# Kernel tuning notes

Hardware: AMD Instinct MI355X
Metric: run time of the kernel (lower is better)

Reference implementation:

```python
import jax, jax.numpy as jnp
import numpy as np

N = 50000
IN, HID, OUT, HEADS = 128, 64, 64, 4


def seg_softmax(logits, seg, num):
    # softmax over edges grouped by destination node; logits [E, H]
    m = jax.ops.segment_max(logits, seg, num_segments=num)
    e = jnp.exp(logits - m[seg])
    s = jax.ops.segment_sum(e, seg, num_segments=num)
    return e / (s[seg] + 1e-16)


def gat_conv(x, src, dst, W, a_s, a_d, b, heads, concat):
    n = x.shape[0]
    h = (x @ W.T).reshape(n, heads, -1)           # [N, H, C]
    alpha_src = jnp.einsum('nhc,hc->nh', h, a_s)   # per-node src score
    alpha_dst = jnp.einsum('nhc,hc->nh', h, a_d)
    logits = jax.nn.leaky_relu(alpha_src[src] + alpha_dst[dst], 0.2)  # [E, H]
    alpha = seg_softmax(logits, dst, n)
    out = jax.ops.segment_sum(alpha[:, :, None] * h[src], dst, num_segments=n)  # [N, H, C]
    out = out.reshape(n, -1) if concat else out.mean(axis=1)
    return out + b


def setup_inputs():
    key = jax.random.key(0)
    ks = jax.random.split(key, 16)
    x = jax.random.normal(ks[0], (N, IN), dtype=jnp.float32)
    edge_index = jax.random.randint(ks[1], (2, 800000), 0, N, dtype=jnp.int64)

    def glorot(k, shape):
        fan = shape[-1]
        return jax.random.normal(k, shape, dtype=jnp.float32) / jnp.sqrt(jnp.float32(fan))

    d = {"x": x, "edge_index": edge_index}
    # layer 1: IN -> HID, HEADS heads, concat
    d["W1"] = glorot(ks[2], (HEADS * HID, IN))
    d["as1"] = glorot(ks[3], (HEADS, HID))
    d["ad1"] = glorot(ks[4], (HEADS, HID))
    d["b1"] = jnp.zeros((HEADS * HID,), jnp.float32)
    # layer 2: HID*HEADS -> HID, HEADS heads, concat
    d["W2"] = glorot(ks[5], (HEADS * HID, HEADS * HID))
    d["as2"] = glorot(ks[6], (HEADS, HID))
    d["ad2"] = glorot(ks[7], (HEADS, HID))
    d["b2"] = jnp.zeros((HEADS * HID,), jnp.float32)
    # layer 3: HID*HEADS -> OUT, 1 head
    d["W3"] = glorot(ks[8], (OUT, HEADS * HID))
    d["as3"] = glorot(ks[9], (1, OUT))
    d["ad3"] = glorot(ks[10], (1, OUT))
    d["b3"] = jnp.zeros((OUT,), jnp.float32)
    return d


def reference(x, edge_index, W1, as1, ad1, b1, W2, as2, ad2, b2, W3, as3, ad3, b3):
    # PyG GATConv adds self-loops by default
    loops = jnp.arange(N, dtype=edge_index.dtype)
    src = jnp.concatenate([edge_index[0], loops])
    dst = jnp.concatenate([edge_index[1], loops])

    h = jax.nn.relu(gat_conv(x, src, dst, W1, as1, ad1, b1, HEADS, True))
    h = jax.nn.relu(gat_conv(h, src, dst, W2, as2, ad2, b2, HEADS, True))
    out = gat_conv(h, src, dst, W3, as3, ad3, b3, 1, True)
    return out
```

## Files before the change

kernel.cpp:

```cpp
#include <hip/hip_runtime.h>
#include <hip/hip_bf16.h>
#include <math.h>


typedef __bf16 bf16x8 __attribute__((ext_vector_type(8)));
typedef float f32x4 __attribute__((ext_vector_type(4)));
typedef _Float16 half8v __attribute__((ext_vector_type(8)));

#define QINV 2048.0f
#define QDQ  4.8828125e-4f

__device__ __forceinline__ void gload_lds16(const void* g, void* l) {
  __builtin_amdgcn_global_load_lds(
      (const __attribute__((address_space(1))) unsigned int*)g,
      (__attribute__((address_space(3))) unsigned int*)l, 16, 0, 0);
}

__device__ __forceinline__ unsigned int splitf(float a) {
  __hip_bfloat16 h = __float2bfloat16(a);
  float hf = __bfloat162float(h);
  __hip_bfloat16 l = __float2bfloat16(a - hf);
  return (unsigned int)__builtin_bit_cast(unsigned short, h) |
         ((unsigned int)__builtin_bit_cast(unsigned short, l) << 16);
}

__device__ __forceinline__ float leaky02(float l) {
  return (l >= 0.f) ? l : 0.2f * l;
}

__device__ __forceinline__ short quant16(float v) {
  int q = (int)rintf(v * QINV);
  q = q > 32767 ? 32767 : (q < -32768 ? -32768 : q);
  return (short)q;
}


__global__ void init_counts_kernel(int* counts, int n) {
  int i = blockIdx.x * blockDim.x + threadIdx.x;
  if (i < n) counts[i] = 1;
}

__global__ void hist_kernel(const int* __restrict__ dst, int e, int* counts) {
  int i = blockIdx.x * blockDim.x + threadIdx.x;
  if (i < e) atomicAdd(&counts[dst[i]], 1);
}

__global__ __launch_bounds__(1024) void block_sum_kernel(const int* __restrict__ counts,
                                                         int* __restrict__ bsum, int n) {
  __shared__ int red[1024];
  int i = blockIdx.x * 1024 + threadIdx.x;
  red[threadIdx.x] = (i < n) ? counts[i] : 0;
  __syncthreads();
  #pragma unroll
  for (int off = 512; off > 0; off >>= 1) {
    if (threadIdx.x < off) red[threadIdx.x] += red[threadIdx.x + off];
    __syncthreads();
  }
  if (threadIdx.x == 0) bsum[blockIdx.x] = red[0];
}

__global__ void scan_sums_kernel(int* bsum, int nb) {
  int t = threadIdx.x;
  int c = (t < nb) ? bsum[t] : 0;
  int v = c;
  #pragma unroll
  for (int off = 1; off < 64; off <<= 1) {
    int u = __shfl_up(v, off);
    if (t >= off) v += u;
  }
  if (t < nb) bsum[t] = v - c;
}

__global__ __launch_bounds__(1024) void scan_final_kernel(const int* __restrict__ counts,
    const int* __restrict__ bsum, int* __restrict__ offsets, int* __restrict__ cursor, int n) {
  __shared__ int sc[1024];
  int i = blockIdx.x * 1024 + threadIdx.x;
  int c = (i < n) ? counts[i] : 0;
  sc[threadIdx.x] = c;
  __syncthreads();
  for (int off = 1; off < 1024; off <<= 1) {
    int v = 0;
    if (threadIdx.x >= off) v = sc[threadIdx.x - off];
    __syncthreads();
    sc[threadIdx.x] += v;
    __syncthreads();
  }
  int excl = sc[threadIdx.x] - c + bsum[blockIdx.x];
  if (i < n) {
    offsets[i] = excl;
    cursor[i] = excl;
  } else if (i == n) {
    offsets[n] = excl;
  }
}

__global__ void scatter_kernel(const int* __restrict__ src, const int* __restrict__ dst,
                               int e800, int etot, int* cursor, int* __restrict__ ssrc) {
  int i = blockIdx.x * blockDim.x + threadIdx.x;
  if (i >= etot) return;
  int s, d;
  if (i < e800) { s = src[i]; d = dst[i]; }
  else          { s = i - e800; d = s; }
  int pos = atomicAdd(&cursor[d], 1);
  ssrc[pos] = s;
}

__global__ void split_kernel(const float* __restrict__ in, uint4* __restrict__ out, int count4) {
  int i = blockIdx.x * blockDim.x + threadIdx.x;
  if (i >= count4) return;
  float4 v = reinterpret_cast<const float4*>(in)[i];
  uint4 o;
  o.x = splitf(v.x); o.y = splitf(v.y); o.z = splitf(v.z); o.w = splitf(v.w);
  out[i] = o;
}

__global__ void splitW_kernel(const float* __restrict__ W1, const float* __restrict__ W2,
                              const float* __restrict__ W3, uint4* __restrict__ o1,
                              uint4* __restrict__ o2, uint4* __restrict__ o3) {
  int i = blockIdx.x * blockDim.x + threadIdx.x;
  const float* in;
  uint4* out;
  int j;
  if (i < 8192)            { in = W1; out = o1; j = i; }
  else if (i < 8192+16384) { in = W2; out = o2; j = i - 8192; }
  else if (i < 8192+16384+4096) { in = W3; out = o3; j = i - (8192+16384); }
  else return;
  float4 v = reinterpret_cast<const float4*>(in)[j];
  uint4 o;
  o.x = splitf(v.x); o.y = splitf(v.y); o.z = splitf(v.z); o.w = splitf(v.w);
  out[j] = o;
}

template <int KP, int BM, int BN, int WAVES_M, int WAVES_N, int OTOT, int HEADS, bool FP16OUT>
__global__ __launch_bounds__(256) void gemm2_kernel(
    const unsigned short* __restrict__ A, const unsigned short* __restrict__ B,
    void* __restrict__ Cq, const float* __restrict__ a_s, const float* __restrict__ a_d,
    float* __restrict__ asrcO, float* __restrict__ adstO, int M) {
  constexpr int BK = 64;
  constexpr int NK = KP / BK;
  constexpr int MFRAG = BM / WAVES_M / 16;
  constexpr int NFRAG = BN / WAVES_N / 16;
  __shared__ unsigned short As[2][BM * BK];
  __shared__ unsigned short Bs[2][BN * BK];

  const int tid = threadIdx.x;
  const int lane = tid & 63;
  const int wid = tid >> 6;
  const int m0 = blockIdx.x * BM;
  const int o0 = blockIdx.y * BN;

  const int srow = tid >> 3;
  const int scolb = (tid & 7) * 16;
  const int sswz = (srow & 7) << 4;
  const char* aSrc = (const char*)A + (size_t)(m0 + srow) * (KP * 2) + (scolb ^ sswz);
  const char* bSrc = (const char*)B + (size_t)(o0 + srow) * (KP * 2) + (scolb ^ sswz);
  char* aDst0 = (char*)&As[0][0] + wid * 1024;
  char* bDst0 = (char*)&Bs[0][0] + wid * 1024;

  auto stage = [&](int buf, int kt) {
    const size_t ko = (size_t)kt * 128;
    char* ad = aDst0 + buf * (BM * 128);
    #pragma unroll
    for (int i = 0; i < BM / 32; ++i)
      gload_lds16(aSrc + ko + (size_t)i * 32 * (KP * 2), ad + i * 4096);
    char* bd = bDst0 + buf * (BN * 128);
    #pragma unroll
    for (int j = 0; j < BN / 32; ++j)
      gload_lds16(bSrc + ko + (size_t)j * 32 * (KP * 2), bd + j * 4096);
  };

  const int fr = lane & 15;
  const int fg = lane >> 4;
  const int fswz = (fr & 7) << 4;
  const int wm0 = (wid / WAVES_N) * (BM / WAVES_M);
  const int wn0 = (wid % WAVES_N) * (BN / WAVES_N);

  f32x4 acc[MFRAG][NFRAG];
  #pragma unroll
  for (int mi = 0; mi < MFRAG; ++mi)
    #pragma unroll
    for (int ni = 0; ni < NFRAG; ++ni) acc[mi][ni] = (f32x4)0.f;

  stage(0, 0);
  __syncthreads();

  for (int kt = 0; kt < NK; ++kt) {
    const int buf = kt & 1;
    if (kt + 1 < NK) stage(buf ^ 1, kt + 1);
    const char* asB = (const char*)&As[buf][0] + (wm0 + fr) * 128;
    const char* bsB = (const char*)&Bs[buf][0] + (wn0 + fr) * 128;
    #pragma unroll
    for (int kh = 0; kh < 2; ++kh) {
      const int kb = (kh * 64 + fg * 16) ^ fswz;
      bf16x8 af[MFRAG], bfr[NFRAG];
      #pragma unroll
      for (int mi = 0; mi < MFRAG; ++mi)
        af[mi] = *reinterpret_cast<const bf16x8*>(asB + mi * 16 * 128 + kb);
      #pragma unroll
      for (int ni = 0; ni < NFRAG; ++ni)
        bfr[ni] = *reinterpret_cast<const bf16x8*>(bsB + ni * 16 * 128 + kb);
      #pragma unroll
      for (int mi = 0; mi < MFRAG; ++mi)
        #pragma unroll
        for (int ni = 0; ni < NFRAG; ++ni)
          acc[mi][ni] = __builtin_amdgcn_mfma_f32_16x16x32_bf16(af[mi], bfr[ni], acc[mi][ni], 0, 0, 0);
    }
    __syncthreads();
  }

  const int head = (o0 + wn0) >> 6;
  float asl[NFRAG], adl[NFRAG];
  #pragma unroll
  for (int ni = 0; ni < NFRAG; ++ni) {
    int c64 = ni * 16 + fr;
    asl[ni] = a_s[head * 64 + c64];
    adl[ni] = a_d[head * 64 + c64];
  }
  #pragma unroll
  for (int mi = 0; mi < MFRAG; ++mi) {
    #pragma unroll
    for (int r = 0; r < 4; ++r) {
      int row = m0 + wm0 + mi * 16 + fg * 4 + r;
      float ps = 0.f, pd = 0.f;
      #pragma unroll
      for (int ni = 0; ni < NFRAG; ++ni) {
        ps = fmaf(acc[mi][ni][r], asl[ni], ps);
        pd = fmaf(acc[mi][ni][r], adl[ni], pd);
      }
      #pragma unroll
      for (int off = 1; off < 16; off <<= 1) {
        ps += __shfl_xor(ps, off);
        pd += __shfl_xor(pd, off);
      }
      if (row < M) {
        if (fr == 0) {
          asrcO[(size_t)row * HEADS + head] = ps;
          adstO[(size_t)row * HEADS + head] = pd;
        }
        #pragma unroll
        for (int ni = 0; ni < NFRAG; ++ni) {
          size_t ci = (size_t)row * OTOT + o0 + wn0 + ni * 16 + fr;
          if (FP16OUT) ((_Float16*)Cq)[ci] = (_Float16)acc[mi][ni][r];
          else         ((short*)Cq)[ci] = quant16(acc[mi][ni][r]);
        }
      }
    }
  }
}

__global__ __launch_bounds__(256) void aggregate4_kernel(
    const _Float16* __restrict__ hq, const float* __restrict__ asrc,
    const float* __restrict__ adst, const float* __restrict__ bias,
    const int* __restrict__ offsets, const int* __restrict__ ssrc,
    uint4* __restrict__ outp, int n) {
  int wid = threadIdx.x >> 6;
  int lane = threadIdx.x & 63;
  int sub = lane >> 5;
  int hl = lane & 31;
  int node = blockIdx.x * 8 + wid * 2 + sub;
  if (node >= n) return;
  int head = hl >> 3;
  int ch8 = hl * 8;
  float adv = adst[(size_t)node * 4 + head];
  int beg = offsets[node], end = offsets[node + 1];

  float s0 = 0.f, s1 = 0.f, s2 = 0.f, s3 = 0.f;
  float A0[8] = {}, A1[8] = {}, A2[8] = {}, A3[8] = {};
  int e = beg;
  for (; e + 3 < end; e += 4) {
    int c0 = ssrc[e + 0], c1 = ssrc[e + 1], c2 = ssrc[e + 2], c3 = ssrc[e + 3];
    float p0 = __expf(leaky02(asrc[(size_t)c0 * 4 + head] + adv));
    float p1 = __expf(leaky02(asrc[(size_t)c1 * 4 + head] + adv));
    float p2 = __expf(leaky02(asrc[(size_t)c2 * 4 + head] + adv));
    float p3 = __expf(leaky02(asrc[(size_t)c3 * 4 + head] + adv));
    half8v h0 = *reinterpret_cast<const half8v*>(&hq[(size_t)c0 * 256 + ch8]);
    half8v h1 = *reinterpret_cast<const half8v*>(&hq[(size_t)c1 * 256 + ch8]);
    half8v h2 = *reinterpret_cast<const half8v*>(&hq[(size_t)c2 * 256 + ch8]);
    half8v h3 = *reinterpret_cast<const half8v*>(&hq[(size_t)c3 * 256 + ch8]);
    s0 += p0; s1 += p1; s2 += p2; s3 += p3;
    #pragma unroll
    for (int j = 0; j < 8; ++j) {
      A0[j] = fmaf((float)h0[j], p0, A0[j]);
      A1[j] = fmaf((float)h1[j], p1, A1[j]);
      A2[j] = fmaf((float)h2[j], p2, A2[j]);
      A3[j] = fmaf((float)h3[j], p3, A3[j]);
    }
  }
  for (; e < end; ++e) {
    int c0 = ssrc[e];
    float p0 = __expf(leaky02(asrc[(size_t)c0 * 4 + head] + adv));
    half8v h0 = *reinterpret_cast<const half8v*>(&hq[(size_t)c0 * 256 + ch8]);
    s0 += p0;
    #pragma unroll
    for (int j = 0; j < 8; ++j) A0[j] = fmaf((float)h0[j], p0, A0[j]);
  }
  float s = (s0 + s1) + (s2 + s3);
  float A[8];
  #pragma unroll
  for (int j = 0; j < 8; ++j) A[j] = (A0[j] + A1[j]) + (A2[j] + A3[j]);

  float inv = 1.f / (s + 1e-16f);
  float4 bv0 = *reinterpret_cast<const float4*>(&bias[ch8]);
  float4 bv1 = *reinterpret_cast<const float4*>(&bias[ch8 + 4]);
  float o[8];
  o[0] = fmaxf(A[0] * inv + bv0.x, 0.f);
  o[1] = fmaxf(A[1] * inv + bv0.y, 0.f);
  o[2] = fmaxf(A[2] * inv + bv0.z, 0.f);
  o[3] = fmaxf(A[3] * inv + bv0.w, 0.f);
  o[4] = fmaxf(A[4] * inv + bv1.x, 0.f);
  o[5] = fmaxf(A[5] * inv + bv1.y, 0.f);
  o[6] = fmaxf(A[6] * inv + bv1.z, 0.f);
  o[7] = fmaxf(A[7] * inv + bv1.w, 0.f);
  uint4 pk0, pk1;
  pk0.x = splitf(o[0]); pk0.y = splitf(o[1]); pk0.z = splitf(o[2]); pk0.w = splitf(o[3]);
  pk1.x = splitf(o[4]); pk1.y = splitf(o[5]); pk1.z = splitf(o[6]); pk1.w = splitf(o[7]);
  outp[(size_t)node * 64 + hl * 2 + 0] = pk0;
  outp[(size_t)node * 64 + hl * 2 + 1] = pk1;
}

__global__ __launch_bounds__(256) void aggregate1_kernel(
    const short* __restrict__ hq, const float* __restrict__ asrc,
    const float* __restrict__ adst, const float* __restrict__ bias,
    const int* __restrict__ offsets, const int* __restrict__ ssrc,
    float* __restrict__ out, int n) {
  int wid = threadIdx.x >> 6;
  int lane = threadIdx.x & 63;
  int node = blockIdx.x * 4 + wid;
  if (node >= n) return;
  int g = lane >> 4;
  int w = lane & 15;
  float adv = adst[node];
  int beg = offsets[node], end = offsets[node + 1];

  float s = 0.f;
  float4 A = {0, 0, 0, 0};
  int e0 = beg;
  for (; e0 + 3 < end; e0 += 4) {
    int src = ssrc[e0 + g];
    float p = __expf(leaky02(asrc[src] + adv));
    short4 q = *reinterpret_cast<const short4*>(&hq[(size_t)src * 64 + w * 4]);
    s += p;
    A.x += p * (float)q.x; A.y += p * (float)q.y;
    A.z += p * (float)q.z; A.w += p * (float)q.w;
  }
  if (e0 + g < end) {
    int src = ssrc[e0 + g];
    float p = __expf(leaky02(asrc[src] + adv));
    short4 q = *reinterpret_cast<const short4*>(&hq[(size_t)src * 64 + w * 4]);
    s += p;
    A.x += p * (float)q.x; A.y += p * (float)q.y;
    A.z += p * (float)q.z; A.w += p * (float)q.w;
  }
  #pragma unroll
  for (int off = 16; off < 64; off <<= 1) {
    s += __shfl_xor(s, off);
    A.x += __shfl_xor(A.x, off);
    A.y += __shfl_xor(A.y, off);
    A.z += __shfl_xor(A.z, off);
    A.w += __shfl_xor(A.w, off);
  }
  if (g == 0) {
    float inv = QDQ / (s + 1e-16f);
    float4 bv = *reinterpret_cast<const float4*>(&bias[w * 4]);
    float4 o;
    o.x = A.x * inv + bv.x;
    o.y = A.y * inv + bv.y;
    o.z = A.z * inv + bv.z;
    o.w = A.w * inv + bv.w;
    *reinterpret_cast<float4*>(&out[(size_t)node * 64 + w * 4]) = o;
  }
}


extern "C" void kernel_launch(void* const* d_in, const int* in_sizes, int n_in,
                              void* d_out, int out_size, void* d_ws, size_t ws_size,
                              hipStream_t stream) {
  const float* x   = (const float*)d_in[0];
  const int*   ei  = (const int*)d_in[1];
  const float* W1  = (const float*)d_in[2];
  const float* as1 = (const float*)d_in[3];
  const float* ad1 = (const float*)d_in[4];
  const float* b1  = (const float*)d_in[5];
  const float* W2  = (const float*)d_in[6];
  const float* as2 = (const float*)d_in[7];
  const float* ad2 = (const float*)d_in[8];
  const float* b2  = (const float*)d_in[9];
  const float* W3  = (const float*)d_in[10];
  const float* as3 = (const float*)d_in[11];
  const float* ad3 = (const float*)d_in[12];
  const float* b3  = (const float*)d_in[13];
  float* out = (float*)d_out;

  const int n    = in_sizes[0] / 128;
  const int e800 = in_sizes[1] / 2;
  const int etot = e800 + n;
  const int Mpad = 50048;

  char* ws = (char*)d_ws;
  size_t off = 0;
  auto alloc = [&](size_t bytes) -> void* {
    void* p = ws + off;
    off = (off + bytes + 255) & ~(size_t)255;
    return p;
  };
  void*           featQ  = alloc((size_t)Mpad * 256 * 2);
  unsigned short* hsplit = (unsigned short*)alloc((size_t)Mpad * 512 * 2);
  unsigned short* w1s    = (unsigned short*)alloc((size_t)256 * 256 * 2);
  unsigned short* w2s    = (unsigned short*)alloc((size_t)256 * 512 * 2);
  unsigned short* w3s    = (unsigned short*)alloc((size_t)64 * 512 * 2);
  float* asrc    = (float*)alloc((size_t)n * 4 * 4);
  float* adst    = (float*)alloc((size_t)n * 4 * 4);
  int*   ssrc    = (int*)alloc((size_t)etot * 4);
  int*   offsets = (int*)alloc((size_t)(n + 1) * 4);
  int*   cursor  = (int*)alloc((size_t)n * 4);
  int*   counts  = (int*)alloc((size_t)n * 4);
  int*   bsum    = (int*)alloc((size_t)64 * 4);

  const int* esrc = ei;
  const int* edst = ei + e800;
  const int nbScan = (n + 1024) / 1024;

  init_counts_kernel<<<(n + 255) / 256, 256, 0, stream>>>(counts, n);
  hist_kernel<<<(e800 + 255) / 256, 256, 0, stream>>>(edst, e800, counts);
  block_sum_kernel<<<nbScan, 1024, 0, stream>>>(counts, bsum, n);
  scan_sums_kernel<<<1, 64, 0, stream>>>(bsum, nbScan);
  scan_final_kernel<<<nbScan, 1024, 0, stream>>>(counts, bsum, offsets, cursor, n);
  scatter_kernel<<<(etot + 255) / 256, 256, 0, stream>>>(esrc, edst, e800, etot, cursor, ssrc);

  split_kernel<<<(n * 128 / 4 + 255) / 256, 256, 0, stream>>>(x, (uint4*)hsplit, n * 128 / 4);
  splitW_kernel<<<(8192 + 16384 + 4096 + 255) / 256, 256, 0, stream>>>(
      W1, W2, W3, (uint4*)w1s, (uint4*)w2s, (uint4*)w3s);

  const int mBlocks = Mpad / 128;

  gemm2_kernel<256, 128, 128, 2, 2, 256, 4, true><<<dim3(mBlocks, 2), 256, 0, stream>>>(
      hsplit, w1s, featQ, as1, ad1, asrc, adst, n);
  aggregate4_kernel<<<(n + 7) / 8, 256, 0, stream>>>(
      (const _Float16*)featQ, asrc, adst, b1, offsets, ssrc, (uint4*)hsplit, n);

  gemm2_kernel<512, 128, 128, 2, 2, 256, 4, true><<<dim3(mBlocks, 2), 256, 0, stream>>>(
      hsplit, w2s, featQ, as2, ad2, asrc, adst, n);
  aggregate4_kernel<<<(n + 7) / 8, 256, 0, stream>>>(
      (const _Float16*)featQ, asrc, adst, b2, offsets, ssrc, (uint4*)hsplit, n);

  gemm2_kernel<512, 128, 64, 4, 1, 64, 1, false><<<dim3(mBlocks, 1), 256, 0, stream>>>(
      hsplit, w3s, featQ, as3, ad3, asrc, adst, n);
  aggregate1_kernel<<<(n + 3) / 4, 256, 0, stream>>>(
      (const short*)featQ, asrc, adst, b3, offsets, ssrc, out, n);
}
```

Baseline: 353.0 us.

## Replace split-bf16 GEMM operands with single fp16 and fuse conversion kernels

```diff
diff --git a/kernel.cpp b/kernel.cpp
--- a/kernel.cpp
+++ b/kernel.cpp
@@ -3,10 +3,11 @@
 #include <math.h>
 
 
-typedef __bf16 bf16x8 __attribute__((ext_vector_type(8)));
 typedef float f32x4 __attribute__((ext_vector_type(4)));
 typedef _Float16 half8v __attribute__((ext_vector_type(8)));
-
+typedef _Float16 half4v __attribute__((ext_vector_type(4)));
+
+#define MPAD 50048
 #define QINV 2048.0f
 #define QDQ  4.8828125e-4f
 
@@ -16,14 +17,6 @@
       (__attribute__((address_space(3))) unsigned int*)l, 16, 0, 0);
 }
 
-__device__ __forceinline__ unsigned int splitf(float a) {
-  __hip_bfloat16 h = __float2bfloat16(a);
-  float hf = __bfloat162float(h);
-  __hip_bfloat16 l = __float2bfloat16(a - hf);
-  return (unsigned int)__builtin_bit_cast(unsigned short, h) |
-         ((unsigned int)__builtin_bit_cast(unsigned short, l) << 16);
-}
-
 __device__ __forceinline__ float leaky02(float l) {
   return (l >= 0.f) ? l : 0.2f * l;
 }
@@ -35,11 +28,6 @@
 }
 
 
-__global__ void init_counts_kernel(int* counts, int n) {
-  int i = blockIdx.x * blockDim.x + threadIdx.x;
-  if (i < n) counts[i] = 1;
-}
-
 __global__ void hist_kernel(const int* __restrict__ dst, int e, int* counts) {
   int i = blockIdx.x * blockDim.x + threadIdx.x;
   if (i < e) atomicAdd(&counts[dst[i]], 1);
@@ -49,7 +37,7 @@
                                                          int* __restrict__ bsum, int n) {
   __shared__ int red[1024];
   int i = blockIdx.x * 1024 + threadIdx.x;
-  red[threadIdx.x] = (i < n) ? counts[i] : 0;
+  red[threadIdx.x] = (i < n) ? (counts[i] + 1) : 0;
   __syncthreads();
   #pragma unroll
   for (int off = 512; off > 0; off >>= 1) {
@@ -75,7 +63,7 @@
     const int* __restrict__ bsum, int* __restrict__ offsets, int* __restrict__ cursor, int n) {
   __shared__ int sc[1024];
   int i = blockIdx.x * 1024 + threadIdx.x;
-  int c = (i < n) ? counts[i] : 0;
+  int c = (i < n) ? (counts[i] + 1) : 0;
   sc[threadIdx.x] = c;
   __syncthreads();
   for (int off = 1; off < 1024; off <<= 1) {
@@ -105,43 +93,35 @@
   ssrc[pos] = s;
 }
 
-__global__ void split_kernel(const float* __restrict__ in, uint4* __restrict__ out, int count4) {
-  int i = blockIdx.x * blockDim.x + threadIdx.x;
-  if (i >= count4) return;
-  float4 v = reinterpret_cast<const float4*>(in)[i];
-  uint4 o;
-  o.x = splitf(v.x); o.y = splitf(v.y); o.z = splitf(v.z); o.w = splitf(v.w);
-  out[i] = o;
-}
-
-__global__ void splitW_kernel(const float* __restrict__ W1, const float* __restrict__ W2,
-                              const float* __restrict__ W3, uint4* __restrict__ o1,
-                              uint4* __restrict__ o2, uint4* __restrict__ o3) {
+__global__ void cvt_all_kernel(const float* __restrict__ x, const float* __restrict__ W1,
+                               const float* __restrict__ W2, const float* __restrict__ W3,
+                               _Float16* __restrict__ x16, _Float16* __restrict__ o1,
+                               _Float16* __restrict__ o2, _Float16* __restrict__ o3, int nx4) {
   int i = blockIdx.x * blockDim.x + threadIdx.x;
   const float* in;
-  uint4* out;
+  _Float16* out;
   int j;
-  if (i < 8192)            { in = W1; out = o1; j = i; }
-  else if (i < 8192+16384) { in = W2; out = o2; j = i - 8192; }
-  else if (i < 8192+16384+4096) { in = W3; out = o3; j = i - (8192+16384); }
+  if (i < nx4)                       { in = x;  out = x16; j = i; }
+  else if ((j = i - nx4) < 8192)     { in = W1; out = o1; }
+  else if ((j -= 8192) < 16384)      { in = W2; out = o2; }
+  else if ((j -= 16384) < 4096)      { in = W3; out = o3; }
   else return;
   float4 v = reinterpret_cast<const float4*>(in)[j];
-  uint4 o;
-  o.x = splitf(v.x); o.y = splitf(v.y); o.z = splitf(v.z); o.w = splitf(v.w);
-  out[j] = o;
-}
-
-template <int KP, int BM, int BN, int WAVES_M, int WAVES_N, int OTOT, int HEADS, bool FP16OUT>
+  half4v h = {(_Float16)v.x, (_Float16)v.y, (_Float16)v.z, (_Float16)v.w};
+  *reinterpret_cast<half4v*>(out + (size_t)j * 4) = h;
+}
+
+template <int KP, int BM, int BN, int WAVES_M, int WAVES_N, int OTOT, int HEADS, bool F16OUT>
 __global__ __launch_bounds__(256) void gemm2_kernel(
-    const unsigned short* __restrict__ A, const unsigned short* __restrict__ B,
+    const _Float16* __restrict__ A, const _Float16* __restrict__ B,
     void* __restrict__ Cq, const float* __restrict__ a_s, const float* __restrict__ a_d,
     float* __restrict__ asrcO, float* __restrict__ adstO, int M) {
   constexpr int BK = 64;
   constexpr int NK = KP / BK;
   constexpr int MFRAG = BM / WAVES_M / 16;
   constexpr int NFRAG = BN / WAVES_N / 16;
-  __shared__ unsigned short As[2][BM * BK];
-  __shared__ unsigned short Bs[2][BN * BK];
+  __shared__ _Float16 As[2][BM * BK];
+  __shared__ _Float16 Bs[2][BN * BK];
 
   const int tid = threadIdx.x;
   const int lane = tid & 63;
@@ -192,27 +172,27 @@
     #pragma unroll
     for (int kh = 0; kh < 2; ++kh) {
       const int kb = (kh * 64 + fg * 16) ^ fswz;
-      bf16x8 af[MFRAG], bfr[NFRAG];
+      half8v af[MFRAG], bfr[NFRAG];
       #pragma unroll
       for (int mi = 0; mi < MFRAG; ++mi)
-        af[mi] = *reinterpret_cast<const bf16x8*>(asB + mi * 16 * 128 + kb);
+        af[mi] = *reinterpret_cast<const half8v*>(asB + mi * 16 * 128 + kb);
       #pragma unroll
       for (int ni = 0; ni < NFRAG; ++ni)
-        bfr[ni] = *reinterpret_cast<const bf16x8*>(bsB + ni * 16 * 128 + kb);
+        bfr[ni] = *reinterpret_cast<const half8v*>(bsB + ni * 16 * 128 + kb);
       #pragma unroll
       for (int mi = 0; mi < MFRAG; ++mi)
         #pragma unroll
         for (int ni = 0; ni < NFRAG; ++ni)
-          acc[mi][ni] = __builtin_amdgcn_mfma_f32_16x16x32_bf16(af[mi], bfr[ni], acc[mi][ni], 0, 0, 0);
+          acc[mi][ni] = __builtin_amdgcn_mfma_f32_16x16x32_f16(af[mi], bfr[ni], acc[mi][ni], 0, 0, 0);
     }
     __syncthreads();
   }
 
-  const int head = (o0 + wn0) >> 6;
+  const int head = (HEADS == 4) ? ((o0 + wn0) >> 6) : 0;
   float asl[NFRAG], adl[NFRAG];
   #pragma unroll
   for (int ni = 0; ni < NFRAG; ++ni) {
-    int c64 = ni * 16 + fr;
+    int c64 = (HEADS == 4) ? (ni * 16 + fr) : (wn0 + ni * 16 + fr);
     asl[ni] = a_s[head * 64 + c64];
     adl[ni] = a_d[head * 64 + c64];
   }
@@ -240,8 +220,8 @@
         #pragma unroll
         for (int ni = 0; ni < NFRAG; ++ni) {
           size_t ci = (size_t)row * OTOT + o0 + wn0 + ni * 16 + fr;
-          if (FP16OUT) ((_Float16*)Cq)[ci] = (_Float16)acc[mi][ni][r];
-          else         ((short*)Cq)[ci] = quant16(acc[mi][ni][r]);
+          if constexpr (F16OUT) ((_Float16*)Cq)[ci] = (_Float16)acc[mi][ni][r];
+          else                  ((short*)Cq)[ci] = quant16(acc[mi][ni][r]);
         }
       }
     }
@@ -252,7 +232,7 @@
     const _Float16* __restrict__ hq, const float* __restrict__ asrc,
     const float* __restrict__ adst, const float* __restrict__ bias,
     const int* __restrict__ offsets, const int* __restrict__ ssrc,
-    uint4* __restrict__ outp, int n) {
+    _Float16* __restrict__ outp, int n) {
   int wid = threadIdx.x >> 6;
   int lane = threadIdx.x & 63;
   int sub = lane >> 5;
@@ -302,20 +282,16 @@
   float inv = 1.f / (s + 1e-16f);
   float4 bv0 = *reinterpret_cast<const float4*>(&bias[ch8]);
   float4 bv1 = *reinterpret_cast<const float4*>(&bias[ch8 + 4]);
-  float o[8];
-  o[0] = fmaxf(A[0] * inv + bv0.x, 0.f);
-  o[1] = fmaxf(A[1] * inv + bv0.y, 0.f);
-  o[2] = fmaxf(A[2] * inv + bv0.z, 0.f);
-  o[3] = fmaxf(A[3] * inv + bv0.w, 0.f);
-  o[4] = fmaxf(A[4] * inv + bv1.x, 0.f);
-  o[5] = fmaxf(A[5] * inv + bv1.y, 0.f);
-  o[6] = fmaxf(A[6] * inv + bv1.z, 0.f);
-  o[7] = fmaxf(A[7] * inv + bv1.w, 0.f);
-  uint4 pk0, pk1;
-  pk0.x = splitf(o[0]); pk0.y = splitf(o[1]); pk0.z = splitf(o[2]); pk0.w = splitf(o[3]);
-  pk1.x = splitf(o[4]); pk1.y = splitf(o[5]); pk1.z = splitf(o[6]); pk1.w = splitf(o[7]);
-  outp[(size_t)node * 64 + hl * 2 + 0] = pk0;
-  outp[(size_t)node * 64 + hl * 2 + 1] = pk1;
+  half8v hv;
+  hv[0] = (_Float16)fmaxf(A[0] * inv + bv0.x, 0.f);
+  hv[1] = (_Float16)fmaxf(A[1] * inv + bv0.y, 0.f);
+  hv[2] = (_Float16)fmaxf(A[2] * inv + bv0.z, 0.f);
+  hv[3] = (_Float16)fmaxf(A[3] * inv + bv0.w, 0.f);
+  hv[4] = (_Float16)fmaxf(A[4] * inv + bv1.x, 0.f);
+  hv[5] = (_Float16)fmaxf(A[5] * inv + bv1.y, 0.f);
+  hv[6] = (_Float16)fmaxf(A[6] * inv + bv1.z, 0.f);
+  hv[7] = (_Float16)fmaxf(A[7] * inv + bv1.w, 0.f);
+  *reinterpret_cast<half8v*>(outp + (size_t)node * 256 + ch8) = hv;
 }
 
 __global__ __launch_bounds__(256) void aggregate1_kernel(
@@ -394,7 +370,6 @@
   const int n    = in_sizes[0] / 128;
   const int e800 = in_sizes[1] / 2;
   const int etot = e800 + n;
-  const int Mpad = 50048;
 
   char* ws = (char*)d_ws;
   size_t off = 0;
@@ -403,14 +378,16 @@
     off = (off + bytes + 255) & ~(size_t)255;
     return p;
   };
-  void*           featQ  = alloc((size_t)Mpad * 256 * 2);
-  unsigned short* hsplit = (unsigned short*)alloc((size_t)Mpad * 512 * 2);
-  unsigned short* w1s    = (unsigned short*)alloc((size_t)256 * 256 * 2);
-  unsigned short* w2s    = (unsigned short*)alloc((size_t)256 * 512 * 2);
-  unsigned short* w3s    = (unsigned short*)alloc((size_t)64 * 512 * 2);
+  _Float16* x16    = (_Float16*)alloc((size_t)MPAD * 128 * 2);
+  _Float16* feat16 = (_Float16*)alloc((size_t)MPAD * 256 * 2);
+  _Float16* hagg16 = (_Float16*)alloc((size_t)MPAD * 256 * 2);
+  short*    featL3 = (short*)alloc((size_t)MPAD * 64 * 2);
+  _Float16* w1f    = (_Float16*)alloc((size_t)256 * 128 * 2);
+  _Float16* w2f    = (_Float16*)alloc((size_t)256 * 256 * 2);
+  _Float16* w3f    = (_Float16*)alloc((size_t)64 * 256 * 2);
   float* asrc    = (float*)alloc((size_t)n * 4 * 4);
   float* adst    = (float*)alloc((size_t)n * 4 * 4);
-  int*   ssrc    = (int*)alloc((size_t)etot * 4);
+  int*   ssrc    = (int*)alloc((size_t)(etot + 4) * 4);
   int*   offsets = (int*)alloc((size_t)(n + 1) * 4);
   int*   cursor  = (int*)alloc((size_t)n * 4);
   int*   counts  = (int*)alloc((size_t)n * 4);
@@ -420,31 +397,31 @@
   const int* edst = ei + e800;
   const int nbScan = (n + 1024) / 1024;
 
-  init_counts_kernel<<<(n + 255) / 256, 256, 0, stream>>>(counts, n);
+  hipMemsetAsync(counts, 0, (size_t)n * 4, stream);
   hist_kernel<<<(e800 + 255) / 256, 256, 0, stream>>>(edst, e800, counts);
   block_sum_kernel<<<nbScan, 1024, 0, stream>>>(counts, bsum, n);
   scan_sums_kernel<<<1, 64, 0, stream>>>(bsum, nbScan);
   scan_final_kernel<<<nbScan, 1024, 0, stream>>>(counts, bsum, offsets, cursor, n);
   scatter_kernel<<<(etot + 255) / 256, 256, 0, stream>>>(esrc, edst, e800, etot, cursor, ssrc);
 
-  split_kernel<<<(n * 128 / 4 + 255) / 256, 256, 0, stream>>>(x, (uint4*)hsplit, n * 128 / 4);
-  splitW_kernel<<<(8192 + 16384 + 4096 + 255) / 256, 256, 0, stream>>>(
-      W1, W2, W3, (uint4*)w1s, (uint4*)w2s, (uint4*)w3s);
-
-  const int mBlocks = Mpad / 128;
+  const int nx4 = n * 128 / 4;
+  cvt_all_kernel<<<(nx4 + 28672 + 255) / 256, 256, 0, stream>>>(
+      x, W1, W2, W3, x16, w1f, w2f, w3f, nx4);
+
+  const int mBlocks = MPAD / 128;
+
+  gemm2_kernel<128, 128, 128, 2, 2, 256, 4, true><<<dim3(mBlocks, 2), 256, 0, stream>>>(
+      x16, w1f, feat16, as1, ad1, asrc, adst, n);
+  aggregate4_kernel<<<(n + 7) / 8, 256, 0, stream>>>(
+      feat16, asrc, adst, b1, offsets, ssrc, hagg16, n);
 
   gemm2_kernel<256, 128, 128, 2, 2, 256, 4, true><<<dim3(mBlocks, 2), 256, 0, stream>>>(
-      hsplit, w1s, featQ, as1, ad1, asrc, adst, n);
+      hagg16, w2f, feat16, as2, ad2, asrc, adst, n);
   aggregate4_kernel<<<(n + 7) / 8, 256, 0, stream>>>(
-      (const _Float16*)featQ, asrc, adst, b1, offsets, ssrc, (uint4*)hsplit, n);
-
-  gemm2_kernel<512, 128, 128, 2, 2, 256, 4, true><<<dim3(mBlocks, 2), 256, 0, stream>>>(
-      hsplit, w2s, featQ, as2, ad2, asrc, adst, n);
-  aggregate4_kernel<<<(n + 7) / 8, 256, 0, stream>>>(
-      (const _Float16*)featQ, asrc, adst, b2, offsets, ssrc, (uint4*)hsplit, n);
-
-  gemm2_kernel<512, 128, 64, 4, 1, 64, 1, false><<<dim3(mBlocks, 1), 256, 0, stream>>>(
-      hsplit, w3s, featQ, as3, ad3, asrc, adst, n);
+      feat16, asrc, adst, b2, offsets, ssrc, hagg16, n);
+
+  gemm2_kernel<256, 128, 64, 4, 1, 64, 1, false><<<dim3(mBlocks, 1), 256, 0, stream>>>(
+      hagg16, w3f, featL3, as3, ad3, asrc, adst, n);
   aggregate1_kernel<<<(n + 3) / 4, 256, 0, stream>>>(
-      (const short*)featQ, asrc, adst, b3, offsets, ssrc, out, n);
-}
+      featL3, asrc, adst, b3, offsets, ssrc, out, n);
+}
```

New measurement: 330.8 us (median of 2 runs). 1.07x faster.
